# Kernel optimization log

Hardware: AMD Instinct MI355X
Metric: run time of the kernel (lower is better)

Reference implementation:

```python
import jax, jax.numpy as jnp
import numpy as np


def _nearest(t, H, W):
    # torch F.interpolate(mode='nearest'): idx = floor(out_i * in/out)
    Hin, Win = t.shape[1], t.shape[2]
    ri = jnp.floor(jnp.arange(H) * (Hin / H)).astype(jnp.int32)
    ci = jnp.floor(jnp.arange(W) * (Win / W)).astype(jnp.int32)
    return t[:, ri][:, :, ci]


def setup_inputs() -> dict:
    key = jax.random.key(0)
    k1, k2, k3, k4 = jax.random.split(key, 4)
    N, A, H, W, C = 4, 256, 256, 256, 19
    features = jax.random.normal(k1, (N, A, H, W), dtype=jnp.float32)
    fc_weight = jax.random.normal(k2, (C, A, 1, 1), dtype=jnp.float32) * 0.05
    y = jax.random.normal(k3, (N, C, H, W), dtype=jnp.float32)
    t = jax.random.randint(k4, (N, 2 * H, 2 * W), 0, 20)
    target_x = jnp.where(t == 19, 255, t).astype(jnp.int32)  # some ignore pixels
    Ave = jnp.zeros((C + 1, A), dtype=jnp.float32)
    CoVariance = jnp.zeros((C + 1, A), dtype=jnp.float32)
    Amount = jnp.zeros((C + 1,), dtype=jnp.float32)
    ratio = jnp.ones((1,), dtype=jnp.float32)
    return {"features": features, "fc_weight": fc_weight, "y": y, "Ave": Ave,
            "CoVariance": CoVariance, "Amount": Amount, "ratio": ratio,
            "target_x": target_x}


def reference(features, fc_weight, y, Ave, CoVariance, Amount, ratio, target_x):
    N, A, H, W = features.shape
    C = fc_weight.shape[0]          # 19 real classes
    Cn = C + 1                      # estimator has an extra ignore slot
    tgt = _nearest(target_x, H, W).reshape(-1)                 # [NHW]
    feat = features.transpose(0, 2, 3, 1).reshape(-1, A)       # [NHW, A]
    y_flat = y.transpose(0, 2, 3, 1).reshape(-1, C)            # [NHW, C]

    # ---- EstimatorCV.update_CV (features detached in original) ----
    f_d = jax.lax.stop_gradient(feat)
    lab_u = jnp.where(tgt == 255, C, tgt)                      # 255 -> class 19
    counts = jax.ops.segment_sum(jnp.ones_like(f_d[:, 0]), lab_u, num_segments=Cn)
    denom = jnp.maximum(counts, 1.0)[:, None]
    ave = jax.ops.segment_sum(f_d, lab_u, num_segments=Cn) / denom        # [Cn,A]
    var = jax.ops.segment_sum((f_d - ave[lab_u]) ** 2, lab_u, num_segments=Cn) / denom
    w = counts / (counts + Amount)
    w = jnp.where(jnp.isnan(w), 0.0, w)[:, None]               # nan (0/0) -> 0
    add_cv = w * (1.0 - w) * (Ave - ave) ** 2
    CoV = CoVariance * (1.0 - w) + var * w + add_cv            # [Cn,A] (detached)
    CoV = jax.lax.stop_gradient(CoV)

    # ---- isda_aug: sigma2[n,c] = ratio * sum_a (W[c]-W[k_n])^2 * CV[k_n] ----
    lab_a = jnp.where(tgt == 255, 0, tgt)
    valid = (tgt != 255).astype(feat.dtype)
    Wm = fc_weight.reshape(C, A)
    Wk = Wm[lab_a]                                             # [NHW, A]
    CVk = CoV[lab_a]                                           # [NHW, A]
    t1 = jnp.einsum('ca,na->nc', Wm * Wm, CVk)
    t2 = jnp.einsum('ca,na->nc', Wm, Wk * CVk)
    t3 = jnp.sum(Wk * Wk * CVk, axis=1, keepdims=True)
    sigma2 = ratio[0] * (t1 - 2.0 * t2 + t3)                   # [NHW, C]
    aug = y_flat + 0.5 * sigma2 * valid[:, None]
    return aug.reshape(N, H, W, C).transpose(0, 3, 1, 2)
```

## Files before the change

kernel.cpp:

```cpp
#include <hip/hip_runtime.h>
#include <hip/hip_bf16.h>
#include <stdint.h>

#define N_IMG 4
#define A_DIM 256
#define HW    65536
#define C_CLS 19
#define NPIX  (N_IMG*HW)
#define CHUNK 512
#define NCHUNK (NPIX/CHUNK)
#define TSPLIT 16

#define OFF_LAB  0
#define OFF_S    262144
#define OFF_HIST 263680
#define OFF_P2   304640
#define OFF_P1   927232
#define P1_ROW_BYTES (C_CLS*2*A_DIM*4)

__device__ __forceinline__ void load_group(float4 (&buf)[8], const float4* f4, int g) {
#pragma unroll
    for (int q = 0; q < 8; ++q) buf[q] = f4[g * 8 + q];
}

__device__ __forceinline__ void proc_group(const float4 (&buf)[8], int g,
                                           const unsigned* labw,
                                           float* __restrict__ s0, float* __restrict__ q0,
                                           float* __restrict__ s1, float* __restrict__ q1,
                                           int t) {
#pragma unroll
    for (int q = 0; q < 8; ++q) {
        unsigned lw = labw[g * 8 + q];
        const float4 vv = buf[q];
#pragma unroll
        for (int i = 0; i < 4; ++i) {
            int lb = (lw >> (8 * i)) & 255;
            float v = (i == 0) ? vv.x : (i == 1) ? vv.y : (i == 2) ? vv.z : vv.w;
            bool ok = lb < C_CLS;
            float vm = ok ? v : 0.0f;
            int row = ok ? lb : 0;
            int idx = (row << 8) + t;
            if (i & 1) {
                s1[idx] += vm;
                q1[idx] = fmaf(vm, vm, q1[idx]);
            } else {
                s0[idx] += vm;
                q0[idx] = fmaf(vm, vm, q0[idx]);
            }
        }
    }
}

__global__ __launch_bounds__(256) void kB_stats(const float* __restrict__ features,
                                                const int* __restrict__ tgt,
                                                uint8_t* __restrict__ lab,
                                                float2* __restrict__ partial,
                                                int* __restrict__ hists, int nblk) {
    __shared__ float s0[C_CLS * A_DIM];
    __shared__ float q0[C_CLS * A_DIM];
    __shared__ float s1[C_CLS * A_DIM];
    __shared__ float q1[C_CLS * A_DIM];
    __shared__ unsigned labw[CHUNK / 4];
    __shared__ int hist[20];
    int t = threadIdx.x;
    for (int i = t; i < C_CLS * A_DIM; i += 256) {
        s0[i] = 0.f; q0[i] = 0.f; s1[i] = 0.f; q1[i] = 0.f;
    }
    if (t < 20) hist[t] = 0;

    for (int ch = blockIdx.x; ch < NCHUNK; ch += nblk) {
        int n = ch >> 7;
        int p0 = (ch & 127) * CHUNK;
        __syncthreads();
        if (t < CHUNK / 4) {
            int p = p0 + t * 4;
            int h = p >> 8, w = p & 255;
            const int* row = tgt + (n << 18) + (h << 10) + (w << 1);
            int4 u0 = *(const int4*)(row);
            int4 u1 = *(const int4*)(row + 4);
            int l0 = (u0.x == 255) ? 19 : u0.x;
            int l1 = (u0.z == 255) ? 19 : u0.z;
            int l2 = (u1.x == 255) ? 19 : u1.x;
            int l3 = (u1.z == 255) ? 19 : u1.z;
            unsigned packed = (unsigned)l0 | ((unsigned)l1 << 8)
                            | ((unsigned)l2 << 16) | ((unsigned)l3 << 24);
            labw[t] = packed;
            ((unsigned*)(lab + n * HW + p0))[t] = packed;
            atomicAdd(&hist[l0], 1); atomicAdd(&hist[l1], 1);
            atomicAdd(&hist[l2], 1); atomicAdd(&hist[l3], 1);
        }
        __syncthreads();

        const float4* f4 = (const float4*)(features + (((size_t)(n * A_DIM + t)) << 16) + p0);
        float4 bufA[8], bufB[8];
        load_group(bufA, f4, 0);
#pragma unroll 1
        for (int g = 0; g < 16; g += 2) {
            load_group(bufB, f4, g + 1);
            proc_group(bufA, g, labw, s0, q0, s1, q1, t);
            if (g + 2 < 16) load_group(bufA, f4, g + 2);
            proc_group(bufB, g + 1, labw, s0, q0, s1, q1, t);
        }
    }
    __syncthreads();
    float2* dst = partial + (size_t)blockIdx.x * (C_CLS * A_DIM);
    for (int i = t; i < C_CLS * A_DIM; i += 256)
        dst[i] = make_float2(s0[i] + s1[i], q0[i] + q1[i]);
    if (t < 20) hists[blockIdx.x * 20 + t] = hist[t];
}

__global__ __launch_bounds__(256) void kC1a(const float2* __restrict__ partial,
                                            float2* __restrict__ p2, int nblk) {
    int c = blockIdx.x;
    int s = blockIdx.y;
    int a = threadIdx.x;
    int per = nblk / TSPLIT;
    float sum = 0.f, sq = 0.f;
    for (int b = s * per; b < (s + 1) * per; ++b) {
        float2 v = partial[(size_t)b * (C_CLS * A_DIM) + c * A_DIM + a];
        sum += v.x; sq += v.y;
    }
    p2[(s * C_CLS + c) * A_DIM + a] = make_float2(sum, sq);
}

__global__ __launch_bounds__(256) void kCF(const float2* __restrict__ p2,
                                           const int* __restrict__ hists, int nblk,
                                           const float* __restrict__ Amount,
                                           const float* __restrict__ Ave,
                                           const float* __restrict__ CoVin,
                                           const float* __restrict__ W,
                                           const float* __restrict__ ratio,
                                           float* __restrict__ S) {
    int k = blockIdx.x, t = threadIdx.x;
    if (k == 19) {
        if (t < C_CLS) S[19 * C_CLS + t] = 0.0f;
        return;
    }
    __shared__ float sred[4];
    __shared__ float red[C_CLS][4];
    int lane = t & 63, wv = t >> 6;
    int csum = 0;
    for (int b = t; b < nblk; b += 256) csum += hists[b * 20 + k];
#pragma unroll
    for (int o = 32; o > 0; o >>= 1) csum += __shfl_xor(csum, o, 64);
    if (lane == 0) sred[wv] = (float)csum;
    __syncthreads();
    float cnt = sred[0] + sred[1] + sred[2] + sred[3];

    float sum = 0.f, sq = 0.f;
#pragma unroll
    for (int s = 0; s < TSPLIT; ++s) {
        float2 v = p2[(s * C_CLS + k) * A_DIM + t];
        sum += v.x; sq += v.y;
    }
    float denom = fmaxf(cnt, 1.0f);
    float ave = sum / denom;
    float var = (sq - 2.0f * ave * sum + ave * ave * cnt) / denom;
    float dw = cnt + Amount[k];
    float w = (dw != 0.0f) ? (cnt / dw) : 0.0f;
    float d = Ave[k * A_DIM + t] - ave;
    float cv = CoVin[k * A_DIM + t] * (1.0f - w) + var * w + w * (1.0f - w) * d * d;

    float wk = W[k * A_DIM + t];
    for (int c = 0; c < C_CLS; ++c) {
        float dd = W[c * A_DIM + t] - wk;
        float term = dd * dd * cv;
#pragma unroll
        for (int o = 32; o > 0; o >>= 1) term += __shfl_xor(term, o, 64);
        if (lane == 0) red[c][wv] = term;
    }
    __syncthreads();
    if (t < C_CLS)
        S[k * C_CLS + t] = 0.5f * ratio[0] * (red[t][0] + red[t][1] + red[t][2] + red[t][3]);
}

__global__ __launch_bounds__(256) void kD_apply(const float* __restrict__ y,
                                                const uint8_t* __restrict__ lab,
                                                const float* __restrict__ S,
                                                float* __restrict__ out) {
    __shared__ float sS[20 * C_CLS];
    int t = threadIdx.x;
    for (int i = t; i < 20 * C_CLS; i += 256) sS[i] = S[i];
    __syncthreads();
    int idx4 = blockIdx.x * 256 + t;
    int plane = idx4 >> 14;
    int p4 = idx4 & 16383;
    int n = plane / C_CLS;
    int c = plane - n * C_CLS;
    float4 yv = ((const float4*)y)[idx4];
    unsigned lw = *(((const unsigned*)(lab + n * HW)) + p4);
    float4 o;
    o.x = yv.x + sS[((lw      ) & 255) * C_CLS + c];
    o.y = yv.y + sS[((lw >> 8 ) & 255) * C_CLS + c];
    o.z = yv.z + sS[((lw >> 16) & 255) * C_CLS + c];
    o.w = yv.w + sS[((lw >> 24)      ) * C_CLS + c];
    ((float4*)out)[idx4] = o;
}

extern "C" void kernel_launch(void* const* d_in, const int* in_sizes, int n_in,
                              void* d_out, int out_size, void* d_ws, size_t ws_size,
                              hipStream_t stream) {
    const float* features  = (const float*)d_in[0];
    const float* fc_weight = (const float*)d_in[1];
    const float* y         = (const float*)d_in[2];
    const float* Ave       = (const float*)d_in[3];
    const float* CoVin     = (const float*)d_in[4];
    const float* Amount    = (const float*)d_in[5];
    const float* ratio     = (const float*)d_in[6];
    const int*   target_x  = (const int*)d_in[7];
    float* out             = (float*)d_out;

    char* ws = (char*)d_ws;
    uint8_t* lab    = (uint8_t*)(ws + OFF_LAB);
    float*   S      = (float*)(ws + OFF_S);
    int*     hists  = (int*)(ws + OFF_HIST);
    float2*  p2     = (float2*)(ws + OFF_P2);
    float2*  partial= (float2*)(ws + OFF_P1);

    size_t avail = (ws_size > (size_t)OFF_P1) ? (ws_size - OFF_P1) : 0;
    int nblk = (int)(avail / P1_ROW_BYTES);
    if (nblk > 512) nblk = 512;
    nblk &= ~15;
    if (nblk < 16) nblk = 16;

    kB_stats<<<nblk, 256, 0, stream>>>(features, target_x, lab, partial, hists, nblk);
    kC1a<<<dim3(C_CLS, TSPLIT), 256, 0, stream>>>(partial, p2, nblk);
    kCF<<<20, 256, 0, stream>>>(p2, hists, nblk, Amount, Ave, CoVin, fc_weight, ratio, S);
    kD_apply<<<(NPIX * C_CLS / 4) / 256, 256, 0, stream>>>(y, lab, S, out);
}
```

Before: 102.1 us.

## Split stats kernel pixel chunk across two thread halves with 512-thread blocks

The feature statistics kernel now launches 512 threads per block instead of 256. Each half of the block processes half of the 512-pixel chunk for the same channel and accumulates into its own shared-memory sum and square buffers. Before, each thread processed the whole chunk and alternated between the two buffer sets. The goal is more memory-level parallelism and more resident waves per block on a kernel bound by memory bandwidth and LDS use. The trade-off is more register pressure under the larger launch bound, and each thread now issues dependent LDS read-modify-writes to a single buffer.

```diff
diff --git a/kernel.cpp b/kernel.cpp
--- a/kernel.cpp
+++ b/kernel.cpp
@@ -24,34 +24,28 @@
 }
 
 __device__ __forceinline__ void proc_group(const float4 (&buf)[8], int g,
-                                           const unsigned* labw,
-                                           float* __restrict__ s0, float* __restrict__ q0,
-                                           float* __restrict__ s1, float* __restrict__ q1,
-                                           int t) {
+                                           const unsigned* lw,
+                                           float* __restrict__ bs,
+                                           float* __restrict__ bq, int ch) {
 #pragma unroll
     for (int q = 0; q < 8; ++q) {
-        unsigned lw = labw[g * 8 + q];
+        unsigned w = lw[g * 8 + q];
         const float4 vv = buf[q];
 #pragma unroll
         for (int i = 0; i < 4; ++i) {
-            int lb = (lw >> (8 * i)) & 255;
+            int lb = (w >> (8 * i)) & 255;
             float v = (i == 0) ? vv.x : (i == 1) ? vv.y : (i == 2) ? vv.z : vv.w;
             bool ok = lb < C_CLS;
             float vm = ok ? v : 0.0f;
             int row = ok ? lb : 0;
-            int idx = (row << 8) + t;
-            if (i & 1) {
-                s1[idx] += vm;
-                q1[idx] = fmaf(vm, vm, q1[idx]);
-            } else {
-                s0[idx] += vm;
-                q0[idx] = fmaf(vm, vm, q0[idx]);
-            }
+            int idx = (row << 8) + ch;
+            bs[idx] += vm;
+            bq[idx] = fmaf(vm, vm, bq[idx]);
         }
     }
 }
 
-__global__ __launch_bounds__(256) void kB_stats(const float* __restrict__ features,
+__global__ __launch_bounds__(512) void kB_stats(const float* __restrict__ features,
                                                 const int* __restrict__ tgt,
                                                 uint8_t* __restrict__ lab,
                                                 float2* __restrict__ partial,
@@ -63,14 +57,17 @@
     __shared__ unsigned labw[CHUNK / 4];
     __shared__ int hist[20];
     int t = threadIdx.x;
-    for (int i = t; i < C_CLS * A_DIM; i += 256) {
+    int ch = t & 255, hf = t >> 8;
+    float* bs = hf ? s1 : s0;
+    float* bq = hf ? q1 : q0;
+    for (int i = t; i < C_CLS * A_DIM; i += 512) {
         s0[i] = 0.f; q0[i] = 0.f; s1[i] = 0.f; q1[i] = 0.f;
     }
     if (t < 20) hist[t] = 0;
 
-    for (int ch = blockIdx.x; ch < NCHUNK; ch += nblk) {
-        int n = ch >> 7;
-        int p0 = (ch & 127) * CHUNK;
+    for (int chk = blockIdx.x; chk < NCHUNK; chk += nblk) {
+        int n = chk >> 7;
+        int p0 = (chk & 127) * CHUNK;
         __syncthreads();
         if (t < CHUNK / 4) {
             int p = p0 + t * 4;
@@ -91,20 +88,22 @@
         }
         __syncthreads();
 
-        const float4* f4 = (const float4*)(features + (((size_t)(n * A_DIM + t)) << 16) + p0);
+        const float4* f4 = (const float4*)(features
+                         + (((size_t)(n * A_DIM + ch)) << 16) + p0 + hf * 256);
+        const unsigned* lw = labw + hf * 64;
         float4 bufA[8], bufB[8];
         load_group(bufA, f4, 0);
 #pragma unroll 1
-        for (int g = 0; g < 16; g += 2) {
+        for (int g = 0; g < 8; g += 2) {
             load_group(bufB, f4, g + 1);
-            proc_group(bufA, g, labw, s0, q0, s1, q1, t);
-            if (g + 2 < 16) load_group(bufA, f4, g + 2);
-            proc_group(bufB, g + 1, labw, s0, q0, s1, q1, t);
+            proc_group(bufA, g, lw, bs, bq, ch);
+            if (g + 2 < 8) load_group(bufA, f4, g + 2);
+            proc_group(bufB, g + 1, lw, bs, bq, ch);
         }
     }
     __syncthreads();
     float2* dst = partial + (size_t)blockIdx.x * (C_CLS * A_DIM);
-    for (int i = t; i < C_CLS * A_DIM; i += 256)
+    for (int i = t; i < C_CLS * A_DIM; i += 512)
         dst[i] = make_float2(s0[i] + s1[i], q0[i] + q1[i]);
     if (t < 20) hists[blockIdx.x * 20 + t] = hist[t];
 }
@@ -223,7 +222,7 @@
     nblk &= ~15;
     if (nblk < 16) nblk = 16;
 
-    kB_stats<<<nblk, 256, 0, stream>>>(features, target_x, lab, partial, hists, nblk);
+    kB_stats<<<nblk, 512, 0, stream>>>(features, target_x, lab, partial, hists, nblk);
     kC1a<<<dim3(C_CLS, TSPLIT), 256, 0, stream>>>(partial, p2, nblk);
     kCF<<<20, 256, 0, stream>>>(p2, hists, nblk, Amount, Ave, CoVin, fc_weight, ratio, S);
     kD_apply<<<(NPIX * C_CLS / 4) / 256, 256, 0, stream>>>(y, lab, S, out);
```

Result: slower. 105.5 us (+3.3%).

## Fuse all four stages into one cooperative kernel with grid syncs

Applied to the files above, without the earlier changes.

Replaces the four separate launches (stats, partial reduce, covariance/sigma, apply) with a single cooperative kernel that separates the phases with grid.sync(). This removes the per-launch overhead and gaps between kernels. In exchange the grid must fit co-resident: each block uses about 78 KB of LDS, which caps it near one block per CU. The apply phase now runs as a grid-stride loop over only nblk blocks instead of a full-width grid, which may lower memory parallelism. If the cooperative launch is rejected, the failure is silently ignored.

```diff
diff --git a/kernel.cpp b/kernel.cpp
--- a/kernel.cpp
+++ b/kernel.cpp
@@ -1,6 +1,9 @@
 #include <hip/hip_runtime.h>
 #include <hip/hip_bf16.h>
+#include <hip/hip_cooperative_groups.h>
 #include <stdint.h>
+
+namespace cg = cooperative_groups;
 
 #define N_IMG 4
 #define A_DIM 256
@@ -24,53 +27,64 @@
 }
 
 __device__ __forceinline__ void proc_group(const float4 (&buf)[8], int g,
-                                           const unsigned* labw,
+                                           const unsigned* lw,
                                            float* __restrict__ s0, float* __restrict__ q0,
                                            float* __restrict__ s1, float* __restrict__ q1,
                                            int t) {
 #pragma unroll
     for (int q = 0; q < 8; ++q) {
-        unsigned lw = labw[g * 8 + q];
+        unsigned w = lw[g * 8 + q];
         const float4 vv = buf[q];
 #pragma unroll
         for (int i = 0; i < 4; ++i) {
-            int lb = (lw >> (8 * i)) & 255;
+            int lb = (w >> (8 * i)) & 255;
             float v = (i == 0) ? vv.x : (i == 1) ? vv.y : (i == 2) ? vv.z : vv.w;
             bool ok = lb < C_CLS;
             float vm = ok ? v : 0.0f;
             int row = ok ? lb : 0;
             int idx = (row << 8) + t;
-            if (i & 1) {
-                s1[idx] += vm;
-                q1[idx] = fmaf(vm, vm, q1[idx]);
-            } else {
-                s0[idx] += vm;
-                q0[idx] = fmaf(vm, vm, q0[idx]);
-            }
-        }
-    }
-}
-
-__global__ __launch_bounds__(256) void kB_stats(const float* __restrict__ features,
-                                                const int* __restrict__ tgt,
-                                                uint8_t* __restrict__ lab,
-                                                float2* __restrict__ partial,
-                                                int* __restrict__ hists, int nblk) {
+            if (i & 1) { s1[idx] += vm; q1[idx] = fmaf(vm, vm, q1[idx]); }
+            else       { s0[idx] += vm; q0[idx] = fmaf(vm, vm, q0[idx]); }
+        }
+    }
+}
+
+__global__ __launch_bounds__(256) void kFused(const float* __restrict__ features,
+                                              const int* __restrict__ tgt,
+                                              uint8_t* __restrict__ lab,
+                                              float2* __restrict__ partial,
+                                              int* __restrict__ hists,
+                                              float2* __restrict__ p2,
+                                              const float* __restrict__ Amount,
+                                              const float* __restrict__ Ave,
+                                              const float* __restrict__ CoVin,
+                                              const float* __restrict__ W,
+                                              const float* __restrict__ ratio,
+                                              float* __restrict__ S,
+                                              const float* __restrict__ y,
+                                              float* __restrict__ out,
+                                              int nblk) {
+    cg::grid_group grid = cg::this_grid();
     __shared__ float s0[C_CLS * A_DIM];
     __shared__ float q0[C_CLS * A_DIM];
     __shared__ float s1[C_CLS * A_DIM];
     __shared__ float q1[C_CLS * A_DIM];
     __shared__ unsigned labw[CHUNK / 4];
     __shared__ int hist[20];
+    __shared__ float sred[4];
+    __shared__ float red[C_CLS][4];
     int t = threadIdx.x;
+    int b = blockIdx.x;
+    int lane = t & 63, wv = t >> 6;
+
     for (int i = t; i < C_CLS * A_DIM; i += 256) {
         s0[i] = 0.f; q0[i] = 0.f; s1[i] = 0.f; q1[i] = 0.f;
     }
     if (t < 20) hist[t] = 0;
 
-    for (int ch = blockIdx.x; ch < NCHUNK; ch += nblk) {
-        int n = ch >> 7;
-        int p0 = (ch & 127) * CHUNK;
+    for (int chk = b; chk < NCHUNK; chk += nblk) {
+        int n = chk >> 7;
+        int p0 = (chk & 127) * CHUNK;
         __syncthreads();
         if (t < CHUNK / 4) {
             int p = p0 + t * 4;
@@ -103,98 +117,92 @@
         }
     }
     __syncthreads();
-    float2* dst = partial + (size_t)blockIdx.x * (C_CLS * A_DIM);
-    for (int i = t; i < C_CLS * A_DIM; i += 256)
-        dst[i] = make_float2(s0[i] + s1[i], q0[i] + q1[i]);
-    if (t < 20) hists[blockIdx.x * 20 + t] = hist[t];
-}
-
-__global__ __launch_bounds__(256) void kC1a(const float2* __restrict__ partial,
-                                            float2* __restrict__ p2, int nblk) {
-    int c = blockIdx.x;
-    int s = blockIdx.y;
-    int a = threadIdx.x;
-    int per = nblk / TSPLIT;
-    float sum = 0.f, sq = 0.f;
-    for (int b = s * per; b < (s + 1) * per; ++b) {
-        float2 v = partial[(size_t)b * (C_CLS * A_DIM) + c * A_DIM + a];
-        sum += v.x; sq += v.y;
-    }
-    p2[(s * C_CLS + c) * A_DIM + a] = make_float2(sum, sq);
-}
-
-__global__ __launch_bounds__(256) void kCF(const float2* __restrict__ p2,
-                                           const int* __restrict__ hists, int nblk,
-                                           const float* __restrict__ Amount,
-                                           const float* __restrict__ Ave,
-                                           const float* __restrict__ CoVin,
-                                           const float* __restrict__ W,
-                                           const float* __restrict__ ratio,
-                                           float* __restrict__ S) {
-    int k = blockIdx.x, t = threadIdx.x;
-    if (k == 19) {
-        if (t < C_CLS) S[19 * C_CLS + t] = 0.0f;
-        return;
-    }
-    __shared__ float sred[4];
-    __shared__ float red[C_CLS][4];
-    int lane = t & 63, wv = t >> 6;
-    int csum = 0;
-    for (int b = t; b < nblk; b += 256) csum += hists[b * 20 + k];
-#pragma unroll
-    for (int o = 32; o > 0; o >>= 1) csum += __shfl_xor(csum, o, 64);
-    if (lane == 0) sred[wv] = (float)csum;
-    __syncthreads();
-    float cnt = sred[0] + sred[1] + sred[2] + sred[3];
-
-    float sum = 0.f, sq = 0.f;
-#pragma unroll
-    for (int s = 0; s < TSPLIT; ++s) {
-        float2 v = p2[(s * C_CLS + k) * A_DIM + t];
-        sum += v.x; sq += v.y;
-    }
-    float denom = fmaxf(cnt, 1.0f);
-    float ave = sum / denom;
-    float var = (sq - 2.0f * ave * sum + ave * ave * cnt) / denom;
-    float dw = cnt + Amount[k];
-    float w = (dw != 0.0f) ? (cnt / dw) : 0.0f;
-    float d = Ave[k * A_DIM + t] - ave;
-    float cv = CoVin[k * A_DIM + t] * (1.0f - w) + var * w + w * (1.0f - w) * d * d;
-
-    float wk = W[k * A_DIM + t];
-    for (int c = 0; c < C_CLS; ++c) {
-        float dd = W[c * A_DIM + t] - wk;
-        float term = dd * dd * cv;
-#pragma unroll
-        for (int o = 32; o > 0; o >>= 1) term += __shfl_xor(term, o, 64);
-        if (lane == 0) red[c][wv] = term;
-    }
-    __syncthreads();
-    if (t < C_CLS)
-        S[k * C_CLS + t] = 0.5f * ratio[0] * (red[t][0] + red[t][1] + red[t][2] + red[t][3]);
-}
-
-__global__ __launch_bounds__(256) void kD_apply(const float* __restrict__ y,
-                                                const uint8_t* __restrict__ lab,
-                                                const float* __restrict__ S,
-                                                float* __restrict__ out) {
-    __shared__ float sS[20 * C_CLS];
-    int t = threadIdx.x;
-    for (int i = t; i < 20 * C_CLS; i += 256) sS[i] = S[i];
-    __syncthreads();
-    int idx4 = blockIdx.x * 256 + t;
-    int plane = idx4 >> 14;
-    int p4 = idx4 & 16383;
-    int n = plane / C_CLS;
-    int c = plane - n * C_CLS;
-    float4 yv = ((const float4*)y)[idx4];
-    unsigned lw = *(((const unsigned*)(lab + n * HW)) + p4);
-    float4 o;
-    o.x = yv.x + sS[((lw      ) & 255) * C_CLS + c];
-    o.y = yv.y + sS[((lw >> 8 ) & 255) * C_CLS + c];
-    o.z = yv.z + sS[((lw >> 16) & 255) * C_CLS + c];
-    o.w = yv.w + sS[((lw >> 24)      ) * C_CLS + c];
-    ((float4*)out)[idx4] = o;
+    {
+        float2* dst = partial + (size_t)b * (C_CLS * A_DIM);
+        for (int i = t; i < C_CLS * A_DIM; i += 256)
+            dst[i] = make_float2(s0[i] + s1[i], q0[i] + q1[i]);
+        if (t < 20) hists[b * 20 + t] = hist[t];
+    }
+    grid.sync();
+
+    {
+        int per = nblk / TSPLIT;
+        for (int u = b; u < C_CLS * TSPLIT; u += nblk) {
+            int c = u >> 4, s = u & 15;
+            float sum = 0.f, sq = 0.f;
+            for (int bb = s * per; bb < (s + 1) * per; ++bb) {
+                float2 v = partial[(size_t)bb * (C_CLS * A_DIM) + c * A_DIM + t];
+                sum += v.x; sq += v.y;
+            }
+            p2[(s * C_CLS + c) * A_DIM + t] = make_float2(sum, sq);
+        }
+    }
+    grid.sync();
+
+    if (b < 20) {
+        int k = b;
+        if (k == 19) {
+            if (t < C_CLS) S[19 * C_CLS + t] = 0.0f;
+        } else {
+            int csum = 0;
+            for (int bb = t; bb < nblk; bb += 256) csum += hists[bb * 20 + k];
+#pragma unroll
+            for (int o = 32; o > 0; o >>= 1) csum += __shfl_xor(csum, o, 64);
+            if (lane == 0) sred[wv] = (float)csum;
+            __syncthreads();
+            float cnt = sred[0] + sred[1] + sred[2] + sred[3];
+
+            float sum = 0.f, sq = 0.f;
+#pragma unroll
+            for (int s = 0; s < TSPLIT; ++s) {
+                float2 v = p2[(s * C_CLS + k) * A_DIM + t];
+                sum += v.x; sq += v.y;
+            }
+            float denom = fmaxf(cnt, 1.0f);
+            float ave = sum / denom;
+            float var = (sq - 2.0f * ave * sum + ave * ave * cnt) / denom;
+            float dw = cnt + Amount[k];
+            float w = (dw != 0.0f) ? (cnt / dw) : 0.0f;
+            float d = Ave[k * A_DIM + t] - ave;
+            float cv = CoVin[k * A_DIM + t] * (1.0f - w) + var * w
+                     + w * (1.0f - w) * d * d;
+
+            float wk = W[k * A_DIM + t];
+            for (int c = 0; c < C_CLS; ++c) {
+                float dd = W[c * A_DIM + t] - wk;
+                float term = dd * dd * cv;
+#pragma unroll
+                for (int o = 32; o > 0; o >>= 1) term += __shfl_xor(term, o, 64);
+                if (lane == 0) red[c][wv] = term;
+            }
+            __syncthreads();
+            if (t < C_CLS)
+                S[k * C_CLS + t] = 0.5f * ratio[0]
+                                 * (red[t][0] + red[t][1] + red[t][2] + red[t][3]);
+        }
+    }
+    grid.sync();
+
+    {
+        float* sS = s0;
+        for (int i = t; i < 20 * C_CLS; i += 256) sS[i] = S[i];
+        __syncthreads();
+        int total4 = NPIX * C_CLS / 4;
+        for (int idx4 = b * 256 + t; idx4 < total4; idx4 += nblk * 256) {
+            int plane = idx4 >> 14;
+            int p4 = idx4 & 16383;
+            int n = plane / C_CLS;
+            int c = plane - n * C_CLS;
+            float4 yv = ((const float4*)y)[idx4];
+            unsigned lw = *(((const unsigned*)(lab + n * HW)) + p4);
+            float4 o;
+            o.x = yv.x + sS[((lw      ) & 255) * C_CLS + c];
+            o.y = yv.y + sS[((lw >> 8 ) & 255) * C_CLS + c];
+            o.z = yv.z + sS[((lw >> 16) & 255) * C_CLS + c];
+            o.w = yv.w + sS[((lw >> 24)      ) * C_CLS + c];
+            ((float4*)out)[idx4] = o;
+        }
+    }
 }
 
 extern "C" void kernel_launch(void* const* d_in, const int* in_sizes, int n_in,
@@ -223,8 +231,10 @@
     nblk &= ~15;
     if (nblk < 16) nblk = 16;
 
-    kB_stats<<<nblk, 256, 0, stream>>>(features, target_x, lab, partial, hists, nblk);
-    kC1a<<<dim3(C_CLS, TSPLIT), 256, 0, stream>>>(partial, p2, nblk);
-    kCF<<<20, 256, 0, stream>>>(p2, hists, nblk, Amount, Ave, CoVin, fc_weight, ratio, S);
-    kD_apply<<<(NPIX * C_CLS / 4) / 256, 256, 0, stream>>>(y, lab, S, out);
-}
+    void* args[] = {(void*)&features, (void*)&target_x, (void*)&lab, (void*)&partial,
+                    (void*)&hists, (void*)&p2, (void*)&Amount, (void*)&Ave,
+                    (void*)&CoVin, (void*)&fc_weight, (void*)&ratio, (void*)&S,
+                    (void*)&y, (void*)&out, (void*)&nblk};
+    (void)hipLaunchCooperativeKernel((void*)kFused, dim3(nblk), dim3(256),
+                                     args, 0, stream);
+}
```

New measurement: 285.0 us. 179% more time.
